# Kernel optimization log

Hardware: AMD Instinct MI355X
Metric: run time of the kernel (lower is better)

Reference implementation:

```python
import jax, jax.numpy as jnp
import numpy as np

EPS = 1e-3  # Keras BatchNormalization default epsilon


def _bn(x, gamma, beta, mean, var):
    # inference-mode batchnorm over channel axis 1 of [N,C,T,V]
    s = (gamma * jax.lax.rsqrt(var + EPS)).reshape(1, -1, 1, 1)
    b = (beta - gamma * mean * jax.lax.rsqrt(var + EPS)).reshape(1, -1, 1, 1)
    return x * s + b


def setup_inputs() -> dict:
    key = jax.random.key(0)
    ks = jax.random.split(key, 10)
    N, C, T, V, K, F, KT = 64, 64, 300, 25, 3, 64, 9
    x = jax.random.normal(ks[0], (N, C, T, V), jnp.float32)
    W1 = jax.random.normal(ks[1], (C, F * K), jnp.float32) * 0.05
    b1 = jnp.zeros((F * K,), jnp.float32)
    A = jax.random.normal(ks[2], (K, T, V, V), jnp.float32) * 0.2
    gamma1 = jnp.ones((F,), jnp.float32)
    beta1 = jnp.zeros((F,), jnp.float32)
    mean1 = jax.random.normal(ks[3], (F,), jnp.float32) * 0.1
    var1 = jax.random.uniform(ks[4], (F,), jnp.float32) + 0.5
    Wt = jax.random.normal(ks[5], (KT, 1, F, F), jnp.float32) * 0.05  # HWIO
    bt = jnp.zeros((F,), jnp.float32)
    gamma2 = jnp.ones((F,), jnp.float32)
    beta2 = jnp.zeros((F,), jnp.float32)
    mean2 = jax.random.normal(ks[6], (F,), jnp.float32) * 0.1
    var2 = jax.random.uniform(ks[7], (F,), jnp.float32) + 0.5
    return dict(x=x, W1=W1, b1=b1, A=A, gamma1=gamma1, beta1=beta1,
                mean1=mean1, var1=var1, Wt=Wt, bt=bt, gamma2=gamma2,
                beta2=beta2, mean2=mean2, var2=var2)


def reference(x, W1, b1, A, gamma1, beta1, mean1, var1, Wt, bt,
              gamma2, beta2, mean2, var2):
    N, C, T, V = x.shape
    K = A.shape[0]
    F = W1.shape[1] // K
    # SGTACN: 1x1 conv (channels_first) == channel matmul
    y = jnp.einsum('nctv,cf->nftv', x, W1) + b1.reshape(1, -1, 1, 1)
    y = y.reshape(N, K, F, T, V)
    # spatial graph contraction with learned per-timestep adjacency
    y = jnp.einsum('nkftv,ktvw->nftw', y, A)
    # tgcn: BN -> relu -> temporal conv [9,1] SAME -> BN
    y = jax.nn.relu(_bn(y, gamma1, beta1, mean1, var1))
    y = jax.lax.conv_general_dilated(
        y, Wt, window_strides=(1, 1), padding='SAME',
        dimension_numbers=('NCHW', 'HWIO', 'NCHW')) + bt.reshape(1, -1, 1, 1)
    y = _bn(y, gamma2, beta2, mean2, var2)
    # identity residual (stride=1, no downsample, C_in == filters) + relu
    return jax.nn.relu(y + x)
```

## Files before the change

### kernel.cpp

```cpp
#include <hip/hip_runtime.h>
#include <hip/hip_bf16.h>
#include <stdint.h>

#define EPS 1e-3f

typedef __attribute__((ext_vector_type(8))) short bf16x8;
typedef __attribute__((ext_vector_type(4))) float f32x4;

__device__ inline uint32_t pk2(float a, float b) {
    __hip_bfloat162 p;
    p.x = __float2bfloat16(a);
    p.y = __float2bfloat16(b);
    return *(uint32_t*)&p;
}

__global__ __launch_bounds__(256) void k0_prep_small(
    const float* __restrict__ W1, const float* __restrict__ Wt,
    const float* __restrict__ A,
    uint16_t* __restrict__ W1t, uint16_t* __restrict__ Abf,
    float* __restrict__ csA_g)
{
    int i = blockIdx.x * 256 + threadIdx.x;
    if (i < 12288) {
        int f = i / 192, Kp = i % 192, k = Kp >> 6, c = Kp & 63;
        __hip_bfloat16 b = __float2bfloat16(W1[c * 192 + k * 64 + f]);
        W1t[i] = *(uint16_t*)&b;
    } else if (i < 49152) {
        int j = i - 12288;
        int jj = j & 7, fo = (j >> 3) & 63, kb = j >> 9;
        int kk = kb * 8 + jj, dt = kk >> 6, fi = kk & 63;
        __hip_bfloat16 b = __float2bfloat16(Wt[(dt * 64 + fi) * 64 + fo]);
        Abf[j] = *(uint16_t*)&b;
    } else if (i < 71652) {
        int j = i - 49152;
        int k = j / 7500, r = j % 7500;
        int t = r / 25, w = r % 25;
        float s = 0.f;
        for (int v = 0; v < 25; ++v)
            s += A[((k * 300 + t) * 25 + v) * 25 + w];
        csA_g[j] = s;
    }
}

__global__ __launch_bounds__(256) void k0_prep_At(
    const float* __restrict__ A, uint16_t* __restrict__ At_g)
{
    int i = blockIdx.x * 256 + threadIdx.x;
    if (i < 921600) {
        int v = i & 31, w = (i >> 5) & 31, rest = i >> 10;
        int t = rest % 300, k = rest / 300;
        float val = 0.f;
        if (v < 25 && w < 25)
            val = A[((k * 300 + t) * 25 + v) * 25 + w];
        __hip_bfloat16 b = __float2bfloat16(val);
        At_g[i] = *(uint16_t*)&b;
    }
}

#define K1_SMEM 39680
__global__ __launch_bounds__(256, 4) void k1_fused(
    const float* __restrict__ x, const uint16_t* __restrict__ At_g,
    const uint16_t* __restrict__ W1t, const float* __restrict__ csA_g,
    const float* __restrict__ b1,
    const float* __restrict__ gamma1, const float* __restrict__ beta1,
    const float* __restrict__ mean1, const float* __restrict__ var1,
    uint32_t* __restrict__ h2u)
{
    extern __shared__ __align__(16) char smem[];
    float* s1s   = (float*)(smem + 38400);
    float* b1ns  = (float*)(smem + 38656);
    float* b1s   = (float*)(smem + 38912);

    const int t0   = blockIdx.x * 4;
    const int n    = blockIdx.y;
    const int tid  = threadIdx.x;
    const int lane = tid & 63, wv = tid >> 6;
    const int l15  = lane & 15, g = lane >> 4;
    const int t    = t0 + wv;

    bf16x8 bfr[6];
    #pragma unroll
    for (int nf = 0; nf < 6; ++nf) {
        const int col = nf * 16 + l15;
        const int k = col >> 5, w = col & 31;
        bfr[nf] = *(const bf16x8*)(At_g + (((k * 300 + t) * 32 + w) * 32 + g * 8));
    }

    const float* xb = x + (size_t)n * 480000 + t * 25;
    bf16x8 a[4];
    #pragma unroll
    for (int mf = 0; mf < 4; ++mf) {
        const int c = l15 + 16 * mf;
        const float* xr = xb + (size_t)c * 7500;
        union { bf16x8 v; uint32_t u[4]; } ua;
        if (g < 3) {
            const float* p = xr + g * 8;
            ua.u[0] = pk2(p[0], p[1]);
            ua.u[1] = pk2(p[2], p[3]);
            ua.u[2] = pk2(p[4], p[5]);
            ua.u[3] = pk2(p[6], p[7]);
        } else {
            ua.u[0] = pk2(xr[24], 0.f);
            ua.u[1] = 0; ua.u[2] = 0; ua.u[3] = 0;
        }
        a[mf] = ua.v;
    }

    if (tid < 64) {
        float rs = rsqrtf(var1[tid] + EPS);
        s1s[tid]  = gamma1[tid] * rs;
        b1ns[tid] = beta1[tid] - gamma1[tid] * mean1[tid] * rs;
    }
    if (tid >= 64 && tid < 256) b1s[tid - 64] = b1[tid - 64];

    f32x4 acc[4][6];
    #pragma unroll
    for (int mf = 0; mf < 4; ++mf)
        #pragma unroll
        for (int nf = 0; nf < 6; ++nf)
            acc[mf][nf] = (f32x4){0.f, 0.f, 0.f, 0.f};

    #pragma unroll
    for (int nf = 0; nf < 6; ++nf) {
        acc[0][nf] = __builtin_amdgcn_mfma_f32_16x16x32_bf16(a[0], bfr[nf], acc[0][nf], 0, 0, 0);
        acc[1][nf] = __builtin_amdgcn_mfma_f32_16x16x32_bf16(a[1], bfr[nf], acc[1][nf], 0, 0, 0);
        acc[2][nf] = __builtin_amdgcn_mfma_f32_16x16x32_bf16(a[2], bfr[nf], acc[2][nf], 0, 0, 0);
        acc[3][nf] = __builtin_amdgcn_mfma_f32_16x16x32_bf16(a[3], bfr[nf], acc[3][nf], 0, 0, 0);
    }

    #pragma unroll
    for (int nf = 0; nf < 6; ++nf) {
        const int col = nf * 16 + l15;
        const int k = col >> 5, w = col & 31;
        if (w < 25) {
            const int colrow = wv * 25 + w;
            const int sw = (w & 7) << 4;
            #pragma unroll
            for (int mf = 0; mf < 4; ++mf) {
                const int c0 = mf * 16 + g * 4;
                const int off = colrow * 384 + (((k * 64 + c0) * 2) ^ sw);
                uint2 val;
                val.x = pk2(acc[mf][nf][0], acc[mf][nf][1]);
                val.y = pk2(acc[mf][nf][2], acc[mf][nf][3]);
                *(uint2*)(smem + off) = val;
            }
        }
    }
    __syncthreads();

    int colv[2], coladdr[2], swz[2];
    const int nq = (wv < 3) ? 2 : 1;
    #pragma unroll
    for (int q = 0; q < 2; ++q) {
        int fr  = wv + 4 * q;
        int col = fr * 16 + l15;
        colv[q] = col;
        int colc = (col < 100) ? col : 99;
        coladdr[q] = colc * 384;
        swz[q] = ((colc % 25) & 7) << 4;
    }

    f32x4 accz[4][2];
    #pragma unroll
    for (int mf = 0; mf < 4; ++mf)
        #pragma unroll
        for (int q = 0; q < 2; ++q)
            accz[mf][q] = (f32x4){0.f, 0.f, 0.f, 0.f};

    #pragma unroll
    for (int kb = 0; kb < 6; ++kb) {
        bf16x8 az[4];
        #pragma unroll
        for (int mf = 0; mf < 4; ++mf)
            az[mf] = *(const bf16x8*)(W1t + (l15 + 16 * mf) * 192 + kb * 32 + g * 8);
        #pragma unroll
        for (int q = 0; q < 2; ++q) {
            if (q < nq) {
                bf16x8 b = *(const bf16x8*)(smem + coladdr[q] + ((kb * 64 + g * 16) ^ swz[q]));
                accz[0][q] = __builtin_amdgcn_mfma_f32_16x16x32_bf16(az[0], b, accz[0][q], 0, 0, 0);
                accz[1][q] = __builtin_amdgcn_mfma_f32_16x16x32_bf16(az[1], b, accz[1][q], 0, 0, 0);
                accz[2][q] = __builtin_amdgcn_mfma_f32_16x16x32_bf16(az[2], b, accz[2][q], 0, 0, 0);
                accz[3][q] = __builtin_amdgcn_mfma_f32_16x16x32_bf16(az[3], b, accz[3][q], 0, 0, 0);
            }
        }
    }

    const uint32_t hbase = (uint32_t)(n * 300 + t0) * 800;
    const int csbase = t0 * 25;
    #pragma unroll
    for (int q = 0; q < 2; ++q) {
        if (q < nq) {
            const int col = colv[q];
            if (col < 100) {
                const int trel = col / 25, w = col - trel * 25;
                const float cs0 = csA_g[csbase + col];
                const float cs1 = csA_g[7500 + csbase + col];
                const float cs2 = csA_g[15000 + csbase + col];
                const uint32_t rowbase = hbase + trel * 800 + w * 32;
                #pragma unroll
                for (int mf = 0; mf < 4; ++mf) {
                    const int f0 = mf * 16 + g * 4;
                    float zz[4];
                    #pragma unroll
                    for (int rg = 0; rg < 4; ++rg) {
                        const int f = f0 + rg;
                        float z = accz[mf][q][rg]
                                + b1s[f] * cs0 + b1s[64 + f] * cs1 + b1s[128 + f] * cs2;
                        z = z * s1s[f] + b1ns[f];
                        zz[rg] = fmaxf(z, 0.f);
                    }
                    uint2 st;
                    st.x = pk2(zz[0], zz[1]);
                    st.y = pk2(zz[2], zz[3]);
                    *(uint2*)(h2u + rowbase + (f0 >> 1)) = st;
                }
            }
        }
    }
}

#define K2_SMEM 77312
__global__ __launch_bounds__(256) void k2_mfma(
    const char* __restrict__ h2b,
    const uint16_t* __restrict__ Abf,
    const float* __restrict__ bt,
    const float* __restrict__ gamma2, const float* __restrict__ beta2,
    const float* __restrict__ mean2,  const float* __restrict__ var2,
    const float* __restrict__ x,
    float* __restrict__ out)
{
    extern __shared__ __align__(16) char smem2[];
    char*  lds_h = smem2;
    float* s2s   = (float*)(smem2 + 76800);
    float* b2s   = s2s + 64;

    const int t0  = blockIdx.x * 16;
    const int n   = blockIdx.y;
    const int tid = threadIdx.x;

    if (tid < 64) {
        float rs = rsqrtf(var2[tid] + EPS);
        float s  = gamma2[tid] * rs;
        s2s[tid] = s;
        b2s[tid] = beta2[tid] - gamma2[tid] * mean2[tid] * rs + bt[tid] * s;
    }

    const size_t hn = (size_t)n * 300 * 3200;
    for (int c = tid; c < 4800; c += 256) {
        int rr = c >> 3, c8 = c & 7;
        int trow = rr / 25;
        int w = rr - trow * 25;
        int tg = t0 - 4 + trow;
        int4 v = make_int4(0, 0, 0, 0);
        if (tg >= 0 && tg < 300)
            v = *(const int4*)(h2b + hn + (size_t)tg * 3200 + w * 128 + (c8 << 4));
        int s = c << 4;
        *(int4*)(lds_h + (s ^ (((s >> 7) & 7) << 4))) = v;
    }
    __syncthreads();

    const int wv = tid >> 6, lane = tid & 63;
    const int l15 = lane & 15, g = lane >> 4;
    const int colbase = wv * 112;
    const int nfr = (wv == 3) ? 4 : 7;

    f32x4 acc[4][7];
    #pragma unroll
    for (int mf = 0; mf < 4; ++mf)
        #pragma unroll
        for (int nf = 0; nf < 7; ++nf)
            acc[mf][nf] = (f32x4){0.f, 0.f, 0.f, 0.f};

    for (int kk = 0; kk < 18; ++kk) {
        const int dt   = kk >> 1;
        const int half = (kk & 1) << 6;
        const int kb   = kk * 4 + g;
        bf16x8 a[4];
        #pragma unroll
        for (int mf = 0; mf < 4; ++mf)
            a[mf] = *(const bf16x8*)(Abf + (kb * 64 + l15 + mf * 16) * 8);
        #pragma unroll
        for (int nf = 0; nf < 7; ++nf) {
            if (nf < nfr) {
                int r = colbase + (nf << 4) + l15 + 25 * dt;
                int s = (r << 7) + half + (g << 4);
                bf16x8 b = *(const bf16x8*)(lds_h + (s ^ ((r & 7) << 4)));
                acc[0][nf] = __builtin_amdgcn_mfma_f32_16x16x32_bf16(a[0], b, acc[0][nf], 0, 0, 0);
                acc[1][nf] = __builtin_amdgcn_mfma_f32_16x16x32_bf16(a[1], b, acc[1][nf], 0, 0, 0);
                acc[2][nf] = __builtin_amdgcn_mfma_f32_16x16x32_bf16(a[2], b, acc[2][nf], 0, 0, 0);
                acc[3][nf] = __builtin_amdgcn_mfma_f32_16x16x32_bf16(a[3], b, acc[3][nf], 0, 0, 0);
            }
        }
    }

    const size_t outn = (size_t)n * 480000;
    #pragma unroll
    for (int mf = 0; mf < 4; ++mf) {
        #pragma unroll
        for (int nf = 0; nf < 7; ++nf) {
            if (nf < nfr) {
                int col  = colbase + (nf << 4) + l15;
                int gcol = t0 * 25 + col;
                if (gcol < 7500) {
                    #pragma unroll
                    for (int reg = 0; reg < 4; ++reg) {
                        int fo = (mf << 4) + (g << 2) + reg;
                        size_t ga = outn + (size_t)fo * 7500 + gcol;
                        float val = acc[mf][nf][reg] * s2s[fo] + b2s[fo];
                        out[ga] = fmaxf(val + x[ga], 0.f);
                    }
                }
            }
        }
    }
}

extern "C" void kernel_launch(void* const* d_in, const int* in_sizes, int n_in,
                              void* d_out, int out_size, void* d_ws, size_t ws_size,
                              hipStream_t stream) {
    const float* x      = (const float*)d_in[0];
    const float* W1     = (const float*)d_in[1];
    const float* b1     = (const float*)d_in[2];
    const float* A      = (const float*)d_in[3];
    const float* gamma1 = (const float*)d_in[4];
    const float* beta1  = (const float*)d_in[5];
    const float* mean1  = (const float*)d_in[6];
    const float* var1   = (const float*)d_in[7];
    const float* Wt     = (const float*)d_in[8];
    const float* bt     = (const float*)d_in[9];
    const float* gamma2 = (const float*)d_in[10];
    const float* beta2  = (const float*)d_in[11];
    const float* mean2  = (const float*)d_in[12];
    const float* var2   = (const float*)d_in[13];
    float* out = (float*)d_out;

    char* ws = (char*)d_ws;
    uint32_t* h2u   = (uint32_t*)ws;
    char*     h2b   = ws;
    uint16_t* At_g  = (uint16_t*)(ws + 61440000);
    uint16_t* W1t   = (uint16_t*)(ws + 63283200);
    uint16_t* Abf   = (uint16_t*)(ws + 63307776);
    float*    csA_g = (float*)   (ws + 63381504);

    hipFuncSetAttribute((const void*)k1_fused,
                        hipFuncAttributeMaxDynamicSharedMemorySize, K1_SMEM);
    hipFuncSetAttribute((const void*)k2_mfma,
                        hipFuncAttributeMaxDynamicSharedMemorySize, K2_SMEM);

    k0_prep_small<<<280, 256, 0, stream>>>(W1, Wt, A, W1t, Abf, csA_g);
    k0_prep_At<<<3600, 256, 0, stream>>>(A, At_g);
    k1_fused<<<dim3(75, 64), 256, K1_SMEM, stream>>>(
        x, At_g, W1t, csA_g, b1, gamma1, beta1, mean1, var1, h2u);
    k2_mfma<<<dim3(19, 64), 256, K2_SMEM, stream>>>(
        h2b, Abf, bt, gamma2, beta2, mean2, var2, x, out);
}
```

Before: 438.5 us.

## Halve k2 time tile, swap MFMA operands for vectorized float4 epilogue

The temporal-conv kernel now handles 8 timesteps per block instead of 16, which cuts LDS to about 51 KB, doubles the grid, and requests 3 blocks per CU. The MFMA operands are swapped so each lane owns 4 consecutive output columns, letting the residual read and output write use float4 accesses instead of scalar strided ones. Columns are interleaved across waves with clamped row indices. The cost is more halo reloading, because 4-row halos are now shared over 8 rows instead of 16, and a tighter register budget.

```diff
diff --git a/kernel.cpp b/kernel.cpp
--- a/kernel.cpp
+++ b/kernel.cpp
@@ -219,8 +219,8 @@
     }
 }
 
-#define K2_SMEM 77312
-__global__ __launch_bounds__(256) void k2_mfma(
+#define K2_SMEM 51712
+__global__ __launch_bounds__(256, 3) void k2_mfma(
     const char* __restrict__ h2b,
     const uint16_t* __restrict__ Abf,
     const float* __restrict__ bt,
@@ -231,10 +231,10 @@
 {
     extern __shared__ __align__(16) char smem2[];
     char*  lds_h = smem2;
-    float* s2s   = (float*)(smem2 + 76800);
+    float* s2s   = (float*)(smem2 + 51200);
     float* b2s   = s2s + 64;
 
-    const int t0  = blockIdx.x * 16;
+    const int t0  = blockIdx.x * 8;
     const int n   = blockIdx.y;
     const int tid = threadIdx.x;
 
@@ -246,7 +246,7 @@
     }
 
     const size_t hn = (size_t)n * 300 * 3200;
-    for (int c = tid; c < 4800; c += 256) {
+    for (int c = tid; c < 3200; c += 256) {
         int rr = c >> 3, c8 = c & 7;
         int trow = rr / 25;
         int w = rr - trow * 25;
@@ -261,54 +261,64 @@
 
     const int wv = tid >> 6, lane = tid & 63;
     const int l15 = lane & 15, g = lane >> 4;
-    const int colbase = wv * 112;
-    const int nfr = (wv == 3) ? 4 : 7;
-
-    f32x4 acc[4][7];
-    #pragma unroll
-    for (int mf = 0; mf < 4; ++mf)
-        #pragma unroll
-        for (int nf = 0; nf < 7; ++nf)
-            acc[mf][nf] = (f32x4){0.f, 0.f, 0.f, 0.f};
+    const int nMf = (wv == 0) ? 4 : 3;
+
+    int rbase[4];
+    #pragma unroll
+    for (int q = 0; q < 4; ++q) {
+        int col = (q * 4 + wv) * 16 + l15;
+        rbase[q] = (col < 200) ? col : 199;
+    }
+
+    f32x4 acc[4][4];
+    #pragma unroll
+    for (int q = 0; q < 4; ++q)
+        #pragma unroll
+        for (int mf = 0; mf < 4; ++mf)
+            acc[q][mf] = (f32x4){0.f, 0.f, 0.f, 0.f};
 
     for (int kk = 0; kk < 18; ++kk) {
         const int dt   = kk >> 1;
         const int half = (kk & 1) << 6;
         const int kb   = kk * 4 + g;
-        bf16x8 a[4];
+        bf16x8 wfr[4];
         #pragma unroll
         for (int mf = 0; mf < 4; ++mf)
-            a[mf] = *(const bf16x8*)(Abf + (kb * 64 + l15 + mf * 16) * 8);
-        #pragma unroll
-        for (int nf = 0; nf < 7; ++nf) {
-            if (nf < nfr) {
-                int r = colbase + (nf << 4) + l15 + 25 * dt;
+            wfr[mf] = *(const bf16x8*)(Abf + (kb * 64 + l15 + mf * 16) * 8);
+        #pragma unroll
+        for (int q = 0; q < 4; ++q) {
+            if (q < nMf) {
+                int r = rbase[q] + 25 * dt;
                 int s = (r << 7) + half + (g << 4);
-                bf16x8 b = *(const bf16x8*)(lds_h + (s ^ ((r & 7) << 4)));
-                acc[0][nf] = __builtin_amdgcn_mfma_f32_16x16x32_bf16(a[0], b, acc[0][nf], 0, 0, 0);
-                acc[1][nf] = __builtin_amdgcn_mfma_f32_16x16x32_bf16(a[1], b, acc[1][nf], 0, 0, 0);
-                acc[2][nf] = __builtin_amdgcn_mfma_f32_16x16x32_bf16(a[2], b, acc[2][nf], 0, 0, 0);
-                acc[3][nf] = __builtin_amdgcn_mfma_f32_16x16x32_bf16(a[3], b, acc[3][nf], 0, 0, 0);
+                bf16x8 hfr = *(const bf16x8*)(lds_h + (s ^ ((r & 7) << 4)));
+                acc[q][0] = __builtin_amdgcn_mfma_f32_16x16x32_bf16(hfr, wfr[0], acc[q][0], 0, 0, 0);
+                acc[q][1] = __builtin_amdgcn_mfma_f32_16x16x32_bf16(hfr, wfr[1], acc[q][1], 0, 0, 0);
+                acc[q][2] = __builtin_amdgcn_mfma_f32_16x16x32_bf16(hfr, wfr[2], acc[q][2], 0, 0, 0);
+                acc[q][3] = __builtin_amdgcn_mfma_f32_16x16x32_bf16(hfr, wfr[3], acc[q][3], 0, 0, 0);
             }
         }
     }
 
     const size_t outn = (size_t)n * 480000;
-    #pragma unroll
-    for (int mf = 0; mf < 4; ++mf) {
-        #pragma unroll
-        for (int nf = 0; nf < 7; ++nf) {
-            if (nf < nfr) {
-                int col  = colbase + (nf << 4) + l15;
-                int gcol = t0 * 25 + col;
-                if (gcol < 7500) {
-                    #pragma unroll
-                    for (int reg = 0; reg < 4; ++reg) {
-                        int fo = (mf << 4) + (g << 2) + reg;
-                        size_t ga = outn + (size_t)fo * 7500 + gcol;
-                        float val = acc[mf][nf][reg] * s2s[fo] + b2s[fo];
-                        out[ga] = fmaxf(val + x[ga], 0.f);
-                    }
+    const int base = t0 * 25;
+    const int vcols = (7500 - base < 200) ? (7500 - base) : 200;
+    #pragma unroll
+    for (int q = 0; q < 4; ++q) {
+        if (q < nMf) {
+            const int col0 = (q * 4 + wv) * 16 + g * 4;
+            if (col0 < vcols) {
+                #pragma unroll
+                for (int mf = 0; mf < 4; ++mf) {
+                    const int fo = mf * 16 + l15;
+                    const size_t ga = outn + (size_t)fo * 7500 + base + col0;
+                    const float4 xr = *(const float4*)(x + ga);
+                    const float s2 = s2s[fo], b2 = b2s[fo];
+                    float4 o;
+                    o.x = fmaxf(acc[q][mf][0] * s2 + b2 + xr.x, 0.f);
+                    o.y = fmaxf(acc[q][mf][1] * s2 + b2 + xr.y, 0.f);
+                    o.z = fmaxf(acc[q][mf][2] * s2 + b2 + xr.z, 0.f);
+                    o.w = fmaxf(acc[q][mf][3] * s2 + b2 + xr.w, 0.f);
+                    *(float4*)(out + ga) = o;
                 }
             }
         }
@@ -351,6 +361,6 @@
     k0_prep_At<<<3600, 256, 0, stream>>>(A, At_g);
     k1_fused<<<dim3(75, 64), 256, K1_SMEM, stream>>>(
         x, At_g, W1t, csA_g, b1, gamma1, beta1, mean1, var1, h2u);
-    k2_mfma<<<dim3(19, 64), 256, K2_SMEM, stream>>>(
+    k2_mfma<<<dim3(38, 64), 256, K2_SMEM, stream>>>(
         h2b, Abf, bt, gamma2, beta2, mean2, var2, x, out);
 }
```

Result: faster. 422.3 us (-3.7%).
